# Kernel tuning notes

Measured on AMD Instinct MI355X. Metric: run time of the kernel, lower is better.

## Reference

```python
import jax, jax.numpy as jnp
import numpy as np

# Natural-order 4x4 Hadamard matrix (H @ H = 4*I); 2D inverse WHT scale = 1/16.
H4 = np.array([[1, 1, 1, 1],
               [1, -1, 1, -1],
               [1, 1, -1, -1],
               [1, -1, -1, 1]], dtype=np.float32)

B, NH, NW, C, K = 16, 28, 28, 64, 64  # out_channels=192 -> K=64 per branch


def setup_inputs() -> dict:
    key = jax.random.key(0)
    ks = jax.random.split(key, 9)
    d = {}
    for i, n in enumerate(['transIm1', 'transIm2', 'transIm3']):
        d[n] = jax.random.normal(ks[i], (16, B, NH, NW, C), dtype=jnp.float32)
    for i, n in enumerate(['weight1', 'weight2', 'weight3']):
        d[n] = jax.random.normal(ks[3 + i], (16, C, K), dtype=jnp.float32) * 0.05
    for i, n in enumerate(['bias1', 'bias2', 'bias3']):
        d[n] = jax.random.normal(ks[6 + i], (1, 1, 1, K), dtype=jnp.float32) * 0.05
    return d


def _iwht_branch(trans, w, b):
    # Per-WHT-coefficient channel matmul: [16,B,nH,nW,C] x [16,C,K] -> [16,B,nH,nW,K]
    y = jnp.einsum('tbijc,tck->tbijk', trans, w)
    _, Bb, nH, nW, Kk = y.shape
    y = y.reshape(4, 4, Bb, nH, nW, Kk)  # coeff index t = 4*u + v
    h = jnp.asarray(H4, y.dtype)
    # Inverse 2D WHT per 4x4 block, scatter blocks back to pixel grid.
    z = jnp.einsum('pu,qv,uvbijk->bipjqk', h, h, y) * (1.0 / 16.0)
    return z.reshape(Bb, 4 * nH, 4 * nW, Kk) + b


def reference(transIm1, transIm2, transIm3, weight1, weight2, weight3,
              bias1, bias2, bias3):
    out1 = _iwht_branch(transIm1, weight1, bias1)
    out2 = _iwht_branch(transIm2, weight2, bias2)
    out3 = _iwht_branch(transIm3, weight3, bias3)
    return (out1, out2, out3)
```

## Files before the change

kernel.cpp:

```cpp
#include <hip/hip_runtime.h>
#include <hip/hip_bf16.h>


typedef __attribute__((ext_vector_type(8))) short bf16x8;
typedef __attribute__((ext_vector_type(4))) float floatx4;

#define NSITES 12544
#define NTILES 784
#define OUT_PER_BRANCH 12845056
#define WT_ELEMS (3*16*64*64)
#define CHUNK_F (64 * 64)

__device__ __forceinline__ short f32_to_bf16_bits(float f) {
    __hip_bfloat16 h = __float2bfloat16(f);
    return *reinterpret_cast<short*>(&h);
}

__global__ void transpose_weights(const float* __restrict__ w0,
                                  const float* __restrict__ w1,
                                  const float* __restrict__ w2,
                                  __hip_bfloat16* __restrict__ wT) {
    int idx = blockIdx.x * blockDim.x + threadIdx.x;
    if (idx >= WT_ELEMS) return;
    int c  = idx & 63;
    int k  = (idx >> 6) & 63;
    int t  = (idx >> 12) & 15;
    int br = idx >> 16;
    const float* w = (br == 0) ? w0 : ((br == 1) ? w1 : w2);
    wT[idx] = __float2bfloat16(w[(t * 64 + c) * 64 + k]);
}

template <bool USE_WT>
__global__ __launch_bounds__(256, 2) void iwht_kernel(
    const float* __restrict__ x0, const float* __restrict__ x1,
    const float* __restrict__ x2,
    const float* __restrict__ w0, const float* __restrict__ w1,
    const float* __restrict__ w2,
    const __hip_bfloat16* __restrict__ wT,
    const float* __restrict__ b0, const float* __restrict__ b1,
    const float* __restrict__ b2,
    float* __restrict__ out) {
    __shared__ float xs[3][CHUNK_F];

    int bx   = blockIdx.x;
    int br   = bx / NTILES;
    int tile = bx - br * NTILES;
    int lane = threadIdx.x & 63;
    int wave = threadIdx.x >> 6;
    int l15  = lane & 15;
    int quad = lane >> 4;
    int n    = wave * 16 + l15;

    const float* x    = (br == 0) ? x0 : ((br == 1) ? x1 : x2);
    const float* w    = (br == 0) ? w0 : ((br == 1) ? w1 : w2);
    const float* bias = (br == 0) ? b0 : ((br == 1) ? b1 : b2);

    int sub  = lane >> 4;
    int lcol = lane & 15;

    floatx4 acc[16];
#pragma unroll
    for (int t = 0; t < 16; t++) acc[t] = (floatx4){0.f, 0.f, 0.f, 0.f};

    bf16x8 wf[32];
    if (USE_WT) {
#pragma unroll
        for (int t = 0; t < 16; t++) {
            const bf16x8* wv = reinterpret_cast<const bf16x8*>(
                wT + (((size_t)(br * 16 + t) * 64 + n) * 64) + quad * 8);
            wf[2 * t]     = wv[0];
            wf[2 * t + 1] = wv[4];
        }
    } else {
#pragma unroll
        for (int t = 0; t < 16; t++) {
#pragma unroll
            for (int j = 0; j < 8; j++) {
                int c0 = quad * 8 + j;
                wf[2 * t][j]     = f32_to_bf16_bits(w[(t * 64 + c0) * 64 + n]);
                wf[2 * t + 1][j] = f32_to_bf16_bits(w[(t * 64 + c0 + 32) * 64 + n]);
            }
        }
    }
    __builtin_amdgcn_sched_barrier(0);

#define STAGE(g, buf)                                                          \
    {                                                                          \
        _Pragma("unroll") for (int r = 0; r < 4; r++) {                        \
            int s   = 4 * r + sub;                  \
            int col = lcol ^ (s & 7);               \
            const float* gp = x +                                              \
                ((size_t)((g) * 4 + wave) * NSITES + tile * 16 + s) * 64 +     \
                col * 4;                                                       \
            __builtin_amdgcn_global_load_lds(                                  \
                (const __attribute__((address_space(1))) void*)gp,             \
                (__attribute__((address_space(3))) void*)                      \
                    &xs[buf][(wave * 16 + 4 * r) * 64],                        \
                16, 0, 0);                                                     \
        }                                                                      \
    }

#define COMPUTE(g, buf)                                                        \
    {                                                                          \
        int xr7 = l15 & 7;                                                     \
        _Pragma("unroll") for (int tl = 0; tl < 4; tl++) {                     \
            int t = (g) * 4 + tl;                                              \
            const float* rp = &xs[buf][(tl * 16 + l15) * 64];                  \
            floatx4 f0 = *(const floatx4*)(rp + ((quad * 2) ^ xr7) * 4);       \
            floatx4 f1 = *(const floatx4*)(rp + ((quad * 2 + 1) ^ xr7) * 4);   \
            floatx4 f2 = *(const floatx4*)(rp + (((quad * 2) ^ xr7) + 8) * 4); \
            floatx4 f3 = *(const floatx4*)(rp + (((quad * 2 + 1) ^ xr7) + 8) * 4); \
            bf16x8 a0, a1;                                                     \
            _Pragma("unroll") for (int j = 0; j < 4; j++) {                    \
                a0[j]     = f32_to_bf16_bits(f0[j]);                           \
                a0[j + 4] = f32_to_bf16_bits(f1[j]);                           \
                a1[j]     = f32_to_bf16_bits(f2[j]);                           \
                a1[j + 4] = f32_to_bf16_bits(f3[j]);                           \
            }                                                                  \
            acc[t] = __builtin_amdgcn_mfma_f32_16x16x32_bf16(wf[2 * t], a0,    \
                                                             acc[t], 0, 0, 0); \
            acc[t] = __builtin_amdgcn_mfma_f32_16x16x32_bf16(wf[2 * t + 1], a1,\
                                                             acc[t], 0, 0, 0); \
        }                                                                      \
    }

#define WAITV(N)                                                               \
    asm volatile("s_waitcnt vmcnt(" #N ")" ::: "memory");                      \
    __builtin_amdgcn_s_barrier();                                              \
    __builtin_amdgcn_sched_barrier(0);

    STAGE(0, 0);
    STAGE(1, 1);
    STAGE(2, 2);

    WAITV(8);
    COMPUTE(0, 0);
    __builtin_amdgcn_s_barrier();
    __builtin_amdgcn_sched_barrier(0);
    STAGE(3, 0);

    WAITV(8);
    COMPUTE(1, 1);

    WAITV(4);
    COMPUTE(2, 2);

    WAITV(0);
    COMPUTE(3, 0);

#undef STAGE
#undef COMPUTE
#undef WAITV

    int k0   = wave * 16 + quad * 4;
    int site = tile * 16 + l15;
    int b    = site / 784;
    int rem  = site - b * 784;
    int i    = rem / 28;
    int j    = rem - i * 28;
    float* op = out + (size_t)br * OUT_PER_BRANCH +
                (((size_t)(b * 112 + 4 * i)) * 112 + 4 * j) * 64 + k0;
    floatx4 bias4 = *reinterpret_cast<const floatx4*>(bias + k0);

#pragma unroll
    for (int u = 0; u < 4; u++) {
        floatx4 y0 = acc[4 * u + 0], y1 = acc[4 * u + 1];
        floatx4 y2 = acc[4 * u + 2], y3 = acc[4 * u + 3];
        floatx4 A = y0 + y2, Bv = y1 + y3, Cv = y0 - y2, Dv = y1 - y3;
        acc[4 * u + 0] = A + Bv;
        acc[4 * u + 1] = A - Bv;
        acc[4 * u + 2] = Cv + Dv;
        acc[4 * u + 3] = Cv - Dv;
    }

#pragma unroll
    for (int q = 0; q < 4; q++) {
        floatx4 z0 = acc[0 + q], z1 = acc[4 + q], z2 = acc[8 + q], z3 = acc[12 + q];
        floatx4 A = z0 + z2, Bv = z1 + z3, Cv = z0 - z2, Dv = z1 - z3;
        floatx4 o[4];
        o[0] = A + Bv;
        o[1] = A - Bv;
        o[2] = Cv + Dv;
        o[3] = Cv - Dv;
#pragma unroll
        for (int p = 0; p < 4; p++) {
            floatx4 v = o[p] * 0.0625f + bias4;
            *reinterpret_cast<floatx4*>(op + (size_t)(p * 112 + q) * 64) = v;
        }
    }
}

extern "C" void kernel_launch(void* const* d_in, const int* in_sizes, int n_in,
                              void* d_out, int out_size, void* d_ws, size_t ws_size,
                              hipStream_t stream) {
    const float* x0 = (const float*)d_in[0];
    const float* x1 = (const float*)d_in[1];
    const float* x2 = (const float*)d_in[2];
    const float* w0 = (const float*)d_in[3];
    const float* w1 = (const float*)d_in[4];
    const float* w2 = (const float*)d_in[5];
    const float* b0 = (const float*)d_in[6];
    const float* b1 = (const float*)d_in[7];
    const float* b2 = (const float*)d_in[8];
    float* out = (float*)d_out;
    __hip_bfloat16* wT = (__hip_bfloat16*)d_ws;

    bool use_wt = ws_size >= (size_t)WT_ELEMS * sizeof(__hip_bfloat16);
    if (use_wt) {
        transpose_weights<<<(WT_ELEMS + 255) / 256, 256, 0, stream>>>(w0, w1, w2, wT);
        iwht_kernel<true><<<3 * NTILES, 256, 0, stream>>>(x0, x1, x2, w0, w1, w2, wT,
                                                          b0, b1, b2, out);
    } else {
        iwht_kernel<false><<<3 * NTILES, 256, 0, stream>>>(x0, x1, x2, w0, w1, w2, wT,
                                                           b0, b1, b2, out);
    }
}
```

Baseline: 292.5 us.

## Make iwht kernel persistent with cross-tile prefetch pipeline

Replaces one-block-per-tile launch (2352 blocks) with 512 persistent blocks that each loop over a contiguous range of tiles in one branch. Weights are loaded once per block and reused across its tiles. A 4-buffer LDS ring prefetches the next tile's input while the current one is computed, and its output is stored in the same loop. This removes per-block weight-load and prologue overhead and hides load latency across tiles, at the cost of more LDS (64KB per block) and a fixed block count that may not match CU occupancy.

```diff
diff --git a/kernel.cpp b/kernel.cpp
--- a/kernel.cpp
+++ b/kernel.cpp
@@ -10,6 +10,7 @@
 #define OUT_PER_BRANCH 12845056
 #define WT_ELEMS (3*16*64*64)
 #define CHUNK_F (64 * 64)
+#define NBLOCKS 512
 
 __device__ __forceinline__ short f32_to_bf16_bits(float f) {
     __hip_bfloat16 h = __float2bfloat16(f);
@@ -40,28 +41,43 @@
     const float* __restrict__ b0, const float* __restrict__ b1,
     const float* __restrict__ b2,
     float* __restrict__ out) {
-    __shared__ float xs[3][CHUNK_F];
+    __shared__ float xs[4][CHUNK_F];
 
     int bx   = blockIdx.x;
-    int br   = bx / NTILES;
-    int tile = bx - br * NTILES;
     int lane = threadIdx.x & 63;
     int wave = threadIdx.x >> 6;
     int l15  = lane & 15;
     int quad = lane >> 4;
     int n    = wave * 16 + l15;
 
+    int br, bi, nb;
+    if (bx < 171)      { br = 0; bi = bx;       nb = 171; }
+    else if (bx < 342) { br = 1; bi = bx - 171; nb = 171; }
+    else               { br = 2; bi = bx - 342; nb = 170; }
+    int t0 = (bi * NTILES) / nb;
+    int t1 = ((bi + 1) * NTILES) / nb;
+
     const float* x    = (br == 0) ? x0 : ((br == 1) ? x1 : x2);
     const float* w    = (br == 0) ? w0 : ((br == 1) ? w1 : w2);
     const float* bias = (br == 0) ? b0 : ((br == 1) ? b1 : b2);
+    float* outb = out + (size_t)br * OUT_PER_BRANCH;
 
     int sub  = lane >> 4;
     int lcol = lane & 15;
+    int rowoff[4];
+#pragma unroll
+    for (int r = 0; r < 4; r++) {
+        int s = 4 * r + sub;
+        rowoff[r] = s * 64 + ((lcol ^ (s & 7)) << 2);
+    }
+
+    int k0 = wave * 16 + quad * 4;
 
     floatx4 acc[16];
 #pragma unroll
     for (int t = 0; t < 16; t++) acc[t] = (floatx4){0.f, 0.f, 0.f, 0.f};
 
+    floatx4 bias4 = *reinterpret_cast<const floatx4*>(bias + k0);
     bf16x8 wf[32];
     if (USE_WT) {
 #pragma unroll
@@ -84,28 +100,27 @@
     }
     __builtin_amdgcn_sched_barrier(0);
 
-#define STAGE(g, buf)                                                          \
+#define STAGE(tt, g)                                                           \
     {                                                                          \
         _Pragma("unroll") for (int r = 0; r < 4; r++) {                        \
-            int s   = 4 * r + sub;                  \
-            int col = lcol ^ (s & 7);               \
             const float* gp = x +                                              \
-                ((size_t)((g) * 4 + wave) * NSITES + tile * 16 + s) * 64 +     \
-                col * 4;                                                       \
+                (size_t)((g) * 4 + wave) * (NSITES * 64) +                     \
+                (size_t)(tt) * 1024 + rowoff[r];                               \
             __builtin_amdgcn_global_load_lds(                                  \
                 (const __attribute__((address_space(1))) void*)gp,             \
                 (__attribute__((address_space(3))) void*)                      \
-                    &xs[buf][(wave * 16 + 4 * r) * 64],                        \
+                    &xs[g][(wave * 16 + 4 * r) * 64],                          \
                 16, 0, 0);                                                     \
         }                                                                      \
-    }
-
-#define COMPUTE(g, buf)                                                        \
+        __builtin_amdgcn_sched_barrier(0);                                     \
+    }
+
+#define COMPUTE(g)                                                             \
     {                                                                          \
         int xr7 = l15 & 7;                                                     \
         _Pragma("unroll") for (int tl = 0; tl < 4; tl++) {                     \
             int t = (g) * 4 + tl;                                              \
-            const float* rp = &xs[buf][(tl * 16 + l15) * 64];                  \
+            const float* rp = &xs[g][(tl * 16 + l15) * 64];                    \
             floatx4 f0 = *(const floatx4*)(rp + ((quad * 2) ^ xr7) * 4);       \
             floatx4 f1 = *(const floatx4*)(rp + ((quad * 2 + 1) ^ xr7) * 4);   \
             floatx4 f2 = *(const floatx4*)(rp + (((quad * 2) ^ xr7) + 8) * 4); \
@@ -124,70 +139,79 @@
         }                                                                      \
     }
 
+#define STORES(tt)                                                             \
+    {                                                                          \
+        int site = (tt) * 16 + l15;                                            \
+        int bb   = site / 784;                                                 \
+        int rem  = site - bb * 784;                                            \
+        int ii   = rem / 28;                                                   \
+        int jj   = rem - ii * 28;                                              \
+        float* op = outb +                                                     \
+            (((size_t)(bb * 112 + 4 * ii)) * 112 + 4 * jj) * 64 + k0;          \
+        _Pragma("unroll") for (int u = 0; u < 4; u++) {                        \
+            floatx4 y0 = acc[4 * u + 0], y1 = acc[4 * u + 1];                  \
+            floatx4 y2 = acc[4 * u + 2], y3 = acc[4 * u + 3];                  \
+            floatx4 A = y0 + y2, Bv = y1 + y3, Cv = y0 - y2, Dv = y1 - y3;     \
+            acc[4 * u + 0] = A + Bv;                                           \
+            acc[4 * u + 1] = A - Bv;                                           \
+            acc[4 * u + 2] = Cv + Dv;                                          \
+            acc[4 * u + 3] = Cv - Dv;                                          \
+        }                                                                      \
+        _Pragma("unroll") for (int q = 0; q < 4; q++) {                        \
+            floatx4 z0 = acc[0 + q], z1 = acc[4 + q];                          \
+            floatx4 z2 = acc[8 + q], z3 = acc[12 + q];                         \
+            floatx4 A = z0 + z2, Bv = z1 + z3, Cv = z0 - z2, Dv = z1 - z3;     \
+            floatx4 o[4];                                                      \
+            o[0] = A + Bv;                                                     \
+            o[1] = A - Bv;                                                     \
+            o[2] = Cv + Dv;                                                    \
+            o[3] = Cv - Dv;                                                    \
+            _Pragma("unroll") for (int p = 0; p < 4; p++) {                    \
+                floatx4 v = o[p] * 0.0625f + bias4;                            \
+                *reinterpret_cast<floatx4*>(op + (size_t)(p * 112 + q) * 64) = v; \
+            }                                                                  \
+        }                                                                      \
+        _Pragma("unroll") for (int t = 0; t < 16; t++)                         \
+            acc[t] = (floatx4){0.f, 0.f, 0.f, 0.f};                            \
+        __builtin_amdgcn_sched_barrier(0);                                     \
+    }
+
 #define WAITV(N)                                                               \
     asm volatile("s_waitcnt vmcnt(" #N ")" ::: "memory");                      \
     __builtin_amdgcn_s_barrier();                                              \
     __builtin_amdgcn_sched_barrier(0);
 
-    STAGE(0, 0);
-    STAGE(1, 1);
-    STAGE(2, 2);
-
-    WAITV(8);
-    COMPUTE(0, 0);
-    __builtin_amdgcn_s_barrier();
+#define BARSB                                                                  \
+    __builtin_amdgcn_s_barrier();                                              \
     __builtin_amdgcn_sched_barrier(0);
-    STAGE(3, 0);
-
-    WAITV(8);
-    COMPUTE(1, 1);
-
-    WAITV(4);
-    COMPUTE(2, 2);
-
-    WAITV(0);
-    COMPUTE(3, 0);
+
+    STAGE(t0, 0);
+    STAGE(t0, 1);
+    STAGE(t0, 2);
+    STAGE(t0, 3);
+
+    WAITV(12); COMPUTE(0); BARSB; STAGE(t0 + 1, 0);
+    WAITV(12); COMPUTE(1); BARSB; STAGE(t0 + 1, 1);
+    WAITV(12); COMPUTE(2); BARSB; STAGE(t0 + 1, 2);
+    WAITV(12); COMPUTE(3); BARSB; STAGE(t0 + 1, 3); STORES(t0);
+
+    for (int tt = t0 + 1; tt <= t1 - 2; ++tt) {
+        WAITV(28); COMPUTE(0); BARSB; STAGE(tt + 1, 0);
+        WAITV(28); COMPUTE(1); BARSB; STAGE(tt + 1, 1);
+        WAITV(28); COMPUTE(2); BARSB; STAGE(tt + 1, 2);
+        WAITV(28); COMPUTE(3); BARSB; STAGE(tt + 1, 3); STORES(tt);
+    }
+
+    WAITV(28); COMPUTE(0);
+    WAITV(24); COMPUTE(1);
+    WAITV(20); COMPUTE(2);
+    WAITV(16); COMPUTE(3); STORES(t1 - 1);
 
 #undef STAGE
 #undef COMPUTE
+#undef STORES
 #undef WAITV
-
-    int k0   = wave * 16 + quad * 4;
-    int site = tile * 16 + l15;
-    int b    = site / 784;
-    int rem  = site - b * 784;
-    int i    = rem / 28;
-    int j    = rem - i * 28;
-    float* op = out + (size_t)br * OUT_PER_BRANCH +
-                (((size_t)(b * 112 + 4 * i)) * 112 + 4 * j) * 64 + k0;
-    floatx4 bias4 = *reinterpret_cast<const floatx4*>(bias + k0);
-
-#pragma unroll
-    for (int u = 0; u < 4; u++) {
-        floatx4 y0 = acc[4 * u + 0], y1 = acc[4 * u + 1];
-        floatx4 y2 = acc[4 * u + 2], y3 = acc[4 * u + 3];
-        floatx4 A = y0 + y2, Bv = y1 + y3, Cv = y0 - y2, Dv = y1 - y3;
-        acc[4 * u + 0] = A + Bv;
-        acc[4 * u + 1] = A - Bv;
-        acc[4 * u + 2] = Cv + Dv;
-        acc[4 * u + 3] = Cv - Dv;
-    }
-
-#pragma unroll
-    for (int q = 0; q < 4; q++) {
-        floatx4 z0 = acc[0 + q], z1 = acc[4 + q], z2 = acc[8 + q], z3 = acc[12 + q];
-        floatx4 A = z0 + z2, Bv = z1 + z3, Cv = z0 - z2, Dv = z1 - z3;
-        floatx4 o[4];
-        o[0] = A + Bv;
-        o[1] = A - Bv;
-        o[2] = Cv + Dv;
-        o[3] = Cv - Dv;
-#pragma unroll
-        for (int p = 0; p < 4; p++) {
-            floatx4 v = o[p] * 0.0625f + bias4;
-            *reinterpret_cast<floatx4*>(op + (size_t)(p * 112 + q) * 64) = v;
-        }
-    }
+#undef BARSB
 }
 
 extern "C" void kernel_launch(void* const* d_in, const int* in_sizes, int n_in,
@@ -208,10 +232,10 @@
     bool use_wt = ws_size >= (size_t)WT_ELEMS * sizeof(__hip_bfloat16);
     if (use_wt) {
         transpose_weights<<<(WT_ELEMS + 255) / 256, 256, 0, stream>>>(w0, w1, w2, wT);
-        iwht_kernel<true><<<3 * NTILES, 256, 0, stream>>>(x0, x1, x2, w0, w1, w2, wT,
-                                                          b0, b1, b2, out);
+        iwht_kernel<true><<<NBLOCKS, 256, 0, stream>>>(x0, x1, x2, w0, w1, w2, wT,
+                                                       b0, b1, b2, out);
     } else {
-        iwht_kernel<false><<<3 * NTILES, 256, 0, stream>>>(x0, x1, x2, w0, w1, w2, wT,
-                                                           b0, b1, b2, out);
-    }
-}
+        iwht_kernel<false><<<NBLOCKS, 256, 0, stream>>>(x0, x1, x2, w0, w1, w2, wT,
+                                                        b0, b1, b2, out);
+    }
+}
```

Result: slower. 301.0 us (+2.9%).

## Stage all 16 coefficient chunks into LDS up front in two halves

Applied to the files above, without the earlier changes.

Replaces the 3-buffer rotating LDS pipeline with a single 64KB buffer holding all 16 coefficient tiles. Loads are issued in two halves, with compute on the first half overlapping the second half's loads, which removes the mid-loop barrier and buffer reuse. Output stores become nontemporal and the bias load moves earlier. The larger LDS footprint (64KB versus 48KB) may reduce how many blocks fit per CU.

```diff
diff --git a/kernel.cpp b/kernel.cpp
--- a/kernel.cpp
+++ b/kernel.cpp
@@ -9,7 +9,6 @@
 #define NTILES 784
 #define OUT_PER_BRANCH 12845056
 #define WT_ELEMS (3*16*64*64)
-#define CHUNK_F (64 * 64)
 
 __device__ __forceinline__ short f32_to_bf16_bits(float f) {
     __hip_bfloat16 h = __float2bfloat16(f);
@@ -40,7 +39,7 @@
     const float* __restrict__ b0, const float* __restrict__ b1,
     const float* __restrict__ b2,
     float* __restrict__ out) {
-    __shared__ float xs[3][CHUNK_F];
+    __shared__ float xs[16 * 16 * 64];
 
     int bx   = blockIdx.x;
     int br   = bx / NTILES;
@@ -58,10 +57,13 @@
     int sub  = lane >> 4;
     int lcol = lane & 15;
 
+    int k0 = wave * 16 + quad * 4;
+
     floatx4 acc[16];
 #pragma unroll
     for (int t = 0; t < 16; t++) acc[t] = (floatx4){0.f, 0.f, 0.f, 0.f};
 
+    floatx4 bias4 = *reinterpret_cast<const floatx4*>(bias + k0);
     bf16x8 wf[32];
     if (USE_WT) {
 #pragma unroll
@@ -84,28 +86,31 @@
     }
     __builtin_amdgcn_sched_barrier(0);
 
-#define STAGE(g, buf)                                                          \
+#define STAGEHALF(h)                                                           \
     {                                                                          \
-        _Pragma("unroll") for (int r = 0; r < 4; r++) {                        \
-            int s   = 4 * r + sub;                  \
-            int col = lcol ^ (s & 7);               \
-            const float* gp = x +                                              \
-                ((size_t)((g) * 4 + wave) * NSITES + tile * 16 + s) * 64 +     \
-                col * 4;                                                       \
-            __builtin_amdgcn_global_load_lds(                                  \
-                (const __attribute__((address_space(1))) void*)gp,             \
-                (__attribute__((address_space(3))) void*)                      \
-                    &xs[buf][(wave * 16 + 4 * r) * 64],                        \
-                16, 0, 0);                                                     \
+        _Pragma("unroll") for (int g = 2 * (h); g < 2 * (h) + 2; ++g) {        \
+            _Pragma("unroll") for (int r = 0; r < 4; r++) {                    \
+                int s   = 4 * r + sub;              \
+                int col = lcol ^ (s & 7);           \
+                const float* gp = x +                                          \
+                    ((size_t)(g * 4 + wave) * NSITES + tile * 16 + s) * 64 +   \
+                    col * 4;                                                   \
+                __builtin_amdgcn_global_load_lds(                              \
+                    (const __attribute__((address_space(1))) void*)gp,         \
+                    (__attribute__((address_space(3))) void*)                  \
+                        &xs[((g * 4 + wave) * 16 + 4 * r) * 64],               \
+                    16, 0, 0);                                                 \
+            }                                                                  \
         }                                                                      \
-    }
-
-#define COMPUTE(g, buf)                                                        \
+        __builtin_amdgcn_sched_barrier(0);                                     \
+    }
+
+#define COMPUTEHALF(h)                                                         \
     {                                                                          \
         int xr7 = l15 & 7;                                                     \
-        _Pragma("unroll") for (int tl = 0; tl < 4; tl++) {                     \
-            int t = (g) * 4 + tl;                                              \
-            const float* rp = &xs[buf][(tl * 16 + l15) * 64];                  \
+        _Pragma("unroll") for (int tl = 0; tl < 8; tl++) {                     \
+            int t = 8 * (h) + tl;                                              \
+            const float* rp = &xs[(t * 16 + l15) * 64];                        \
             floatx4 f0 = *(const floatx4*)(rp + ((quad * 2) ^ xr7) * 4);       \
             floatx4 f1 = *(const floatx4*)(rp + ((quad * 2 + 1) ^ xr7) * 4);   \
             floatx4 f2 = *(const floatx4*)(rp + (((quad * 2) ^ xr7) + 8) * 4); \
@@ -129,30 +134,19 @@
     __builtin_amdgcn_s_barrier();                                              \
     __builtin_amdgcn_sched_barrier(0);
 
-    STAGE(0, 0);
-    STAGE(1, 1);
-    STAGE(2, 2);
+    STAGEHALF(0);
+    STAGEHALF(1);
 
     WAITV(8);
-    COMPUTE(0, 0);
-    __builtin_amdgcn_s_barrier();
-    __builtin_amdgcn_sched_barrier(0);
-    STAGE(3, 0);
-
-    WAITV(8);
-    COMPUTE(1, 1);
-
-    WAITV(4);
-    COMPUTE(2, 2);
+    COMPUTEHALF(0);
 
     WAITV(0);
-    COMPUTE(3, 0);
-
-#undef STAGE
-#undef COMPUTE
+    COMPUTEHALF(1);
+
+#undef STAGEHALF
+#undef COMPUTEHALF
 #undef WAITV
 
-    int k0   = wave * 16 + quad * 4;
     int site = tile * 16 + l15;
     int b    = site / 784;
     int rem  = site - b * 784;
@@ -160,7 +154,6 @@
     int j    = rem - i * 28;
     float* op = out + (size_t)br * OUT_PER_BRANCH +
                 (((size_t)(b * 112 + 4 * i)) * 112 + 4 * j) * 64 + k0;
-    floatx4 bias4 = *reinterpret_cast<const floatx4*>(bias + k0);
 
 #pragma unroll
     for (int u = 0; u < 4; u++) {
@@ -185,7 +178,8 @@
 #pragma unroll
         for (int p = 0; p < 4; p++) {
             floatx4 v = o[p] * 0.0625f + bias4;
-            *reinterpret_cast<floatx4*>(op + (size_t)(p * 112 + q) * 64) = v;
+            __builtin_nontemporal_store(
+                v, reinterpret_cast<floatx4*>(op + (size_t)(p * 112 + q) * 64));
         }
     }
 }
```

New measurement: 304.2 us. 1.04x slower.
